# Optimization experiments

Hardware: AMD Instinct MI355X
Metric: run time of the kernel (lower is better)

## Reference

```python
import jax, jax.numpy as jnp
import numpy as np

VOCAB = 50000
EMBED = 256
LABELS = 2
DEPTH = 10          # complete binary tree: 2**DEPTH leaves
B = 256             # batch of trees
L = 2 ** DEPTH      # leaves per tree


def setup_inputs() -> dict:
    key = jax.random.key(0)
    ks = jax.random.split(key, 7)
    token_ids = jax.random.randint(ks[0], (B, L), 0, VOCAB)
    labels = jax.random.randint(ks[1], (B,), 0, LABELS)
    emb = jax.random.normal(ks[2], (VOCAB, EMBED), dtype=jnp.float32)
    W_w = jax.random.normal(ks[3], (EMBED, 2 * EMBED), dtype=jnp.float32) * (1.0 / np.sqrt(2 * EMBED))
    W_b = jax.random.normal(ks[4], (EMBED,), dtype=jnp.float32) * 0.01
    P_w = jax.random.normal(ks[5], (LABELS, EMBED), dtype=jnp.float32) * (1.0 / np.sqrt(EMBED))
    P_b = jax.random.normal(ks[6], (LABELS,), dtype=jnp.float32) * 0.01
    return {"token_ids": token_ids, "labels": labels, "emb": emb,
            "W_w": W_w, "W_b": W_b, "P_w": P_w, "P_b": P_b}


def reference(token_ids, labels, emb, W_w, W_b, P_w, P_b):
    # Leaves: relu(embedding(token))  -> [B, L, E]
    x = jax.nn.relu(emb[token_ids])
    # Level-by-level combine: currentNode = relu(W @ cat(left, right) + b)
    # Leaf order is left-to-right, so adjacent pairs (2k, 2k+1) are siblings;
    # reshape concatenates (left, right) along features, matching torch.cat((l, r), 1).
    while x.shape[1] > 1:
        bsz, n, e = x.shape
        lr = x.reshape(bsz, n // 2, 2 * e)                       # [B, n/2, 2E]
        x = jax.nn.relu(jnp.einsum('bnf,ef->bne', lr, W_w) + W_b)
    root = x[:, 0]                                               # [B, E]
    logits = root @ P_w.T + P_b                                  # [B, label_size]
    prediction = jnp.argmax(logits, axis=1)
    logp = jax.nn.log_softmax(logits, axis=-1)
    loss = -jnp.take_along_axis(logp, labels[:, None], axis=1)[:, 0]  # per-tree CE
    return prediction, loss
```

## Files before the change

kernel.cpp:

```cpp
#include <hip/hip_runtime.h>
#include <hip/hip_bf16.h>
#include <math.h>

#define EMBED   256
#define KDIM    512
#define BATCH   256
#define BM      128
#define BN      128

typedef float  f32x4   __attribute__((ext_vector_type(4)));
typedef __bf16 bf16x8  __attribute__((ext_vector_type(8)));
typedef unsigned short ushort8 __attribute__((ext_vector_type(8)));

__device__ __forceinline__ unsigned short f2h(float f) {
    unsigned int u = __float_as_uint(f);
    u += 0x7FFFu + ((u >> 16) & 1u);
    return (unsigned short)(u >> 16);
}
__device__ __forceinline__ float h2f(unsigned short h) {
    return __uint_as_float(((unsigned int)h) << 16);
}
__device__ __forceinline__ void gload16(const void* g, void* l) {
    __builtin_amdgcn_global_load_lds(
        (const __attribute__((address_space(1))) unsigned int*)g,
        (__attribute__((address_space(3))) unsigned int*)l, 16, 0, 0);
}

template<int LV1, int WPREP>
__global__ __launch_bounds__(256) void gemm_tree(
    const unsigned short* __restrict__ Xh, const unsigned short* __restrict__ Xl,
    const unsigned short* __restrict__ Wh, const unsigned short* __restrict__ Wl,
    const float*  __restrict__ Wf,
    const float*  __restrict__ bias,
    unsigned short* __restrict__ Yh, unsigned short* __restrict__ Yl,
    const int* __restrict__ tok, const float* __restrict__ emb)
{
    __shared__ __align__(16) unsigned short AhL[4096], AlL[4096];
    __shared__ __align__(16) unsigned short BhL[4096], BlL[4096];

    const int tid = threadIdx.x;
    const int w   = tid >> 6;
    const int l   = tid & 63;
    const int q   = l >> 4;
    const int rr  = l & 15;

    const int nwg = gridDim.x;
    const int bid = blockIdx.x;
    const int swz = (bid & 7) * (nwg >> 3) + (bid >> 3);
    const int m0  = (swz >> 1) * BM;
    const int n0  = (swz & 1) * BN;

    const int waveM = w >> 1;
    const int waveN = w & 1;

    int tk[2][2];
    if constexpr (LV1) {
        #pragma unroll
        for (int g = 0; g < 2; ++g) {
            const int r = m0 + (w + g * 4) * 16 + rr;
            tk[g][0] = tok[2 * r];
            tk[g][1] = tok[2 * r + 1];
        }
    }

    f32x4 acc[4][4] = {};

    for (int t = 0; t < 16; ++t) {
        const int k0   = t << 5;
        const int joff = k0 >> 8;
        const int c    = (k0 & 255) + q * 8;

        if constexpr (LV1) {
            #pragma unroll
            for (int g = 0; g < 2; ++g) {
                const int s = w + g * 4;
                const float* e = emb + (size_t)tk[g][joff] * EMBED + c;
                float v[8];
                *(float4*)&v[0] = *(const float4*)e;
                *(float4*)&v[4] = *(const float4*)(e + 4);
                ushort8 hs, ls;
                #pragma unroll
                for (int i = 0; i < 8; ++i) {
                    const float f = fmaxf(v[i], 0.f);
                    const unsigned short h = f2h(f);
                    hs[i] = h;
                    ls[i] = f2h(f - h2f(h));
                }
                *(ushort8*)&AhL[s * 512 + l * 8] = hs;
                *(ushort8*)&AlL[s * 512 + l * 8] = ls;
            }
        } else {
            #pragma unroll
            for (int g = 0; g < 2; ++g) {
                const int s = w + g * 4;
                const size_t off = (size_t)(2 * (m0 + s * 16 + rr) + joff) * EMBED + c;
                gload16(Xh + off, &AhL[s * 512]);
                gload16(Xl + off, &AlL[s * 512]);
            }
        }

        #pragma unroll
        for (int g = 0; g < 2; ++g) {
            const int s = w + g * 4;
            if constexpr (WPREP) {
                const size_t off = (size_t)(n0 + s * 16 + rr) * KDIM + k0 + q * 8;
                gload16(Wh + off, &BhL[s * 512]);
                gload16(Wl + off, &BlL[s * 512]);
            } else {
                const float* ws = Wf + (size_t)(n0 + s * 16 + rr) * KDIM + k0 + q * 8;
                float v[8];
                *(float4*)&v[0] = *(const float4*)ws;
                *(float4*)&v[4] = *(const float4*)(ws + 4);
                ushort8 hs, ls;
                #pragma unroll
                for (int i = 0; i < 8; ++i) {
                    const unsigned short h = f2h(v[i]);
                    hs[i] = h;
                    ls[i] = f2h(v[i] - h2f(h));
                }
                *(ushort8*)&BhL[s * 512 + l * 8] = hs;
                *(ushort8*)&BlL[s * 512 + l * 8] = ls;
            }
        }

        __syncthreads();

        bf16x8 a0[4], b0[4], x0[4];
        #pragma unroll
        for (int mi = 0; mi < 4; ++mi)
            a0[mi] = *(const bf16x8*)&AhL[(waveM * 4 + mi) * 512 + l * 8];
        #pragma unroll
        for (int ni = 0; ni < 4; ++ni)
            b0[ni] = *(const bf16x8*)&BhL[(waveN * 4 + ni) * 512 + l * 8];
        #pragma unroll
        for (int mi = 0; mi < 4; ++mi)
            #pragma unroll
            for (int ni = 0; ni < 4; ++ni)
                acc[mi][ni] = __builtin_amdgcn_mfma_f32_16x16x32_bf16(a0[mi], b0[ni], acc[mi][ni], 0, 0, 0);

        #pragma unroll
        for (int ni = 0; ni < 4; ++ni)
            x0[ni] = *(const bf16x8*)&BlL[(waveN * 4 + ni) * 512 + l * 8];
        #pragma unroll
        for (int mi = 0; mi < 4; ++mi)
            #pragma unroll
            for (int ni = 0; ni < 4; ++ni)
                acc[mi][ni] = __builtin_amdgcn_mfma_f32_16x16x32_bf16(a0[mi], x0[ni], acc[mi][ni], 0, 0, 0);

        #pragma unroll
        for (int mi = 0; mi < 4; ++mi)
            x0[mi] = *(const bf16x8*)&AlL[(waveM * 4 + mi) * 512 + l * 8];
        #pragma unroll
        for (int mi = 0; mi < 4; ++mi)
            #pragma unroll
            for (int ni = 0; ni < 4; ++ni)
                acc[mi][ni] = __builtin_amdgcn_mfma_f32_16x16x32_bf16(x0[mi], b0[ni], acc[mi][ni], 0, 0, 0);

        __syncthreads();
    }

    #pragma unroll
    for (int ni = 0; ni < 4; ++ni) {
        const int col = n0 + waveN * 64 + ni * 16 + rr;
        const float bv = bias[col];
        #pragma unroll
        for (int mi = 0; mi < 4; ++mi) {
            const int row0 = m0 + waveM * 64 + mi * 16 + q * 4;
            #pragma unroll
            for (int jj = 0; jj < 4; ++jj) {
                const float y = fmaxf(acc[mi][ni][jj] + bv, 0.f);
                const unsigned short h = f2h(y);
                Yh[(size_t)(row0 + jj) * EMBED + col] = h;
                Yl[(size_t)(row0 + jj) * EMBED + col] = f2h(y - h2f(h));
            }
        }
    }
}

template<int WPREP>
__global__ __launch_bounds__(256) void tail_kernel(
    const unsigned short* __restrict__ Xh5, const unsigned short* __restrict__ Xl5,
    const unsigned short* __restrict__ Wh, const unsigned short* __restrict__ Wl,
    const float* __restrict__ Wf, const float* __restrict__ bias,
    const float* __restrict__ Pw, const float* __restrict__ Pb,
    const int* __restrict__ labels, float* __restrict__ out)
{
    __shared__ __align__(16) unsigned short X0h[8192], X0l[8192];
    __shared__ __align__(16) unsigned short X1h[4096], X1l[4096];
    __shared__ __align__(16) unsigned short BhT[2][8192], BlT[2][8192];

    const int tid = threadIdx.x;
    const int w   = tid >> 6;
    const int l   = tid & 63;
    const int q   = l >> 4;
    const int rr  = l & 15;
    const int b   = blockIdx.x;

    {
        const int row = tid >> 3;
        const int c0  = (tid & 7) * 32;
        #pragma unroll
        for (int i = 0; i < 4; ++i) {
            const int col = c0 + i * 8;
            const int sw  = (row * 256 + col) ^ ((row & 7) << 3);
            *(ushort8*)&X0h[sw] = *(const ushort8*)&Xh5[(size_t)(b * 32 + row) * EMBED + col];
            *(ushort8*)&X0l[sw] = *(const ushort8*)&Xl5[(size_t)(b * 32 + row) * EMBED + col];
        }
    }

    auto stageB = [&](int buf, int k0) {
        if constexpr (WPREP) {
            #pragma unroll
            for (int j = 0; j < 8; ++j) {
                const int sb = w * 8 + j;
                const int s  = sb & 15;
                const size_t off = (size_t)(s * 16 + rr) * KDIM + k0 + q * 8;
                if (sb < 16) gload16(Wh + off, &BhT[buf][s * 512]);
                else         gload16(Wl + off, &BlT[buf][s * 512]);
            }
        } else {
            #pragma unroll
            for (int j = 0; j < 4; ++j) {
                const int u = w * 4 + j;
                const float* ws = Wf + (size_t)(u * 16 + rr) * KDIM + k0 + q * 8;
                float v[8];
                *(float4*)&v[0] = *(const float4*)ws;
                *(float4*)&v[4] = *(const float4*)(ws + 4);
                ushort8 hs, ls;
                #pragma unroll
                for (int i = 0; i < 8; ++i) {
                    const unsigned short h = f2h(v[i]);
                    hs[i] = h;
                    ls[i] = f2h(v[i] - h2f(h));
                }
                *(ushort8*)&BhT[buf][u * 512 + l * 8] = hs;
                *(ushort8*)&BlT[buf][u * 512 + l * 8] = ls;
            }
        }
    };

    float bv[4];
    #pragma unroll
    for (int ni = 0; ni < 4; ++ni) bv[ni] = bias[w * 64 + ni * 16 + rr];

    stageB(0, 0);
    __syncthreads();

    int g = 0;
    for (int lv = 0; lv < 5; ++lv) {
        unsigned short* srch = (lv & 1) ? X1h : X0h;
        unsigned short* srcl = (lv & 1) ? X1l : X0l;
        unsigned short* dsth = (lv & 1) ? X0h : X1h;
        unsigned short* dstl = (lv & 1) ? X0l : X1l;
        const int Mout = 16 >> lv;

        f32x4 acc[4] = {};
        for (int t = 0; t < 16; ++t, ++g) {
            const int cur = g & 1;
            if (g < 79) stageB(cur ^ 1, ((t + 1) & 15) * 32);

            const int k0   = t * 32;
            const int joff = k0 >> 8;
            const int c    = (k0 & 255) + q * 8;
            const int row  = 2 * rr + joff;
            const int idx  = (row * 256 + c) ^ ((row & 7) << 3);
            const bf16x8 a_h = *(const bf16x8*)&srch[idx];
            const bf16x8 a_l = *(const bf16x8*)&srcl[idx];

            bf16x8 bh4[4], bl4[4];
            #pragma unroll
            for (int ni = 0; ni < 4; ++ni) {
                bh4[ni] = *(const bf16x8*)&BhT[cur][(w * 4 + ni) * 512 + l * 8];
                bl4[ni] = *(const bf16x8*)&BlT[cur][(w * 4 + ni) * 512 + l * 8];
            }
            #pragma unroll
            for (int ni = 0; ni < 4; ++ni)
                acc[ni] = __builtin_amdgcn_mfma_f32_16x16x32_bf16(a_h, bh4[ni], acc[ni], 0, 0, 0);
            #pragma unroll
            for (int ni = 0; ni < 4; ++ni)
                acc[ni] = __builtin_amdgcn_mfma_f32_16x16x32_bf16(a_l, bh4[ni], acc[ni], 0, 0, 0);
            #pragma unroll
            for (int ni = 0; ni < 4; ++ni)
                acc[ni] = __builtin_amdgcn_mfma_f32_16x16x32_bf16(a_h, bl4[ni], acc[ni], 0, 0, 0);

            __syncthreads();
        }

        #pragma unroll
        for (int ni = 0; ni < 4; ++ni) {
            const int col = w * 64 + ni * 16 + rr;
            #pragma unroll
            for (int jj = 0; jj < 4; ++jj) {
                const int row = q * 4 + jj;
                if (row < Mout) {
                    const float y = fmaxf(acc[ni][jj] + bv[ni], 0.f);
                    const unsigned short h = f2h(y);
                    const int idx = (row * 256 + col) ^ ((row & 7) << 3);
                    dsth[idx] = h;
                    dstl[idx] = f2h(y - h2f(h));
                }
            }
        }
        __syncthreads();
    }

    if (w == 0) {
        float s0 = 0.f, s1 = 0.f;
        #pragma unroll
        for (int i = 0; i < 4; ++i) {
            const int col = l + i * 64;
            const float x = h2f(X1h[col]) + h2f(X1l[col]);
            s0 = fmaf(x, Pw[col], s0);
            s1 = fmaf(x, Pw[EMBED + col], s1);
        }
        #pragma unroll
        for (int off = 32; off > 0; off >>= 1) {
            s0 += __shfl_down(s0, off);
            s1 += __shfl_down(s1, off);
        }
        if (l == 0) {
            const float l0 = s0 + Pb[0];
            const float l1 = s1 + Pb[1];
            const int pred = (l1 > l0) ? 1 : 0;
            const float m  = fmaxf(l0, l1);
            const float lse = m + logf(expf(l0 - m) + expf(l1 - m));
            const int lab = labels[b];
            out[b]         = (float)pred;
            out[BATCH + b] = lse - (lab ? l1 : l0);
        }
    }
}

__global__ __launch_bounds__(256) void prep_w(const float* __restrict__ W,
                                              unsigned short* __restrict__ Wh,
                                              unsigned short* __restrict__ Wl)
{
    const int i = blockIdx.x * 256 + threadIdx.x;
    const float w = W[i];
    const unsigned short h = f2h(w);
    Wh[i] = h;
    Wl[i] = f2h(w - h2f(h));
}

extern "C" void kernel_launch(void* const* d_in, const int* in_sizes, int n_in,
                              void* d_out, int out_size, void* d_ws, size_t ws_size,
                              hipStream_t stream)
{
    const int*   token_ids = (const int*)d_in[0];
    const int*   labels    = (const int*)d_in[1];
    const float* emb       = (const float*)d_in[2];
    const float* W_w       = (const float*)d_in[3];
    const float* W_b       = (const float*)d_in[4];
    const float* P_w       = (const float*)d_in[5];
    const float* P_b       = (const float*)d_in[6];
    float*       out       = (float*)d_out;

    unsigned short* Ah_buf = (unsigned short*)d_ws;
    unsigned short* Al_buf = Ah_buf + (size_t)131072 * 256;
    unsigned short* Bh_buf = Al_buf + (size_t)131072 * 256;
    unsigned short* Bl_buf = Bh_buf + (size_t)65536 * 256;
    unsigned short* Wh     = Bl_buf + (size_t)65536 * 256;
    unsigned short* Wl     = Wh + 131072;

    const size_t need_wprep = ((size_t)131072 * 256 * 2 + (size_t)65536 * 256 * 2 + 2 * 131072) * 2;
    const bool wprep = ws_size >= need_wprep;

    if (wprep) prep_w<<<512, 256, 0, stream>>>(W_w, Wh, Wl);

    int R = 131072;
    const unsigned short *inh = nullptr, *inl = nullptr;
    for (int lv = 1; lv <= 5; ++lv) {
        unsigned short* yh = (lv & 1) ? Ah_buf : Bh_buf;
        unsigned short* yl = (lv & 1) ? Al_buf : Bl_buf;
        dim3 grid((R / BM) * 2);
        if (lv == 1) {
            if (wprep) gemm_tree<1,1><<<grid, 256, 0, stream>>>(nullptr, nullptr, Wh, Wl, W_w, W_b, yh, yl, token_ids, emb);
            else       gemm_tree<1,0><<<grid, 256, 0, stream>>>(nullptr, nullptr, Wh, Wl, W_w, W_b, yh, yl, token_ids, emb);
        } else {
            if (wprep) gemm_tree<0,1><<<grid, 256, 0, stream>>>(inh, inl, Wh, Wl, W_w, W_b, yh, yl, nullptr, nullptr);
            else       gemm_tree<0,0><<<grid, 256, 0, stream>>>(inh, inl, Wh, Wl, W_w, W_b, yh, yl, nullptr, nullptr);
        }
        inh = yh; inl = yl; R >>= 1;
    }

    if (wprep) tail_kernel<1><<<BATCH, 256, 0, stream>>>(inh, inl, Wh, Wl, W_w, W_b, P_w, P_b, labels, out);
    else       tail_kernel<0><<<BATCH, 256, 0, stream>>>(inh, inl, Wh, Wl, W_w, W_b, P_w, P_b, labels, out);
}
```

Before: 449.6 us.

## Pre-split embedding table, widen GEMM tiles to full N, fold level five into tail

A new prep kernel converts the ReLU'd embedding table into bf16 hi/lo halves once, so the level-1 GEMM can stage A through direct global-to-LDS loads instead of converting in registers. gemm_tree now uses 512-thread blocks covering all 256 output columns per 128-row tile, so each A tile is read once instead of twice. Level 5 moves into the tail kernel, which streams its 64-row input per tree and runs six levels in one launch, removing a kernel launch and an intermediate round trip. The cost is converting the full 50000x256 table each call, a larger per-block LDS footprint, and reuse of the B buffers as embedding storage.

```diff
diff --git a/kernel.cpp b/kernel.cpp
--- a/kernel.cpp
+++ b/kernel.cpp
@@ -6,7 +6,7 @@
 #define KDIM    512
 #define BATCH   256
 #define BM      128
-#define BN      128
+#define VOCAB   50000
 
 typedef float  f32x4   __attribute__((ext_vector_type(4)));
 typedef __bf16 bf16x8  __attribute__((ext_vector_type(8)));
@@ -26,41 +26,65 @@
         (__attribute__((address_space(3))) unsigned int*)l, 16, 0, 0);
 }
 
+__global__ __launch_bounds__(256) void prep_emb(const float* __restrict__ emb,
+                                                unsigned short* __restrict__ Eh,
+                                                unsigned short* __restrict__ El)
+{
+    const size_t base = ((size_t)blockIdx.x * 256 + threadIdx.x) * 8;
+    float v[8];
+    *(float4*)&v[0] = *(const float4*)&emb[base];
+    *(float4*)&v[4] = *(const float4*)&emb[base + 4];
+    ushort8 hs, ls;
+    #pragma unroll
+    for (int i = 0; i < 8; ++i) {
+        const float f = fmaxf(v[i], 0.f);
+        const unsigned short h = f2h(f);
+        hs[i] = h;
+        ls[i] = f2h(f - h2f(h));
+    }
+    *(ushort8*)&Eh[base] = hs;
+    *(ushort8*)&El[base] = ls;
+}
+
+__global__ __launch_bounds__(256) void prep_w(const float* __restrict__ W,
+                                              unsigned short* __restrict__ Wh,
+                                              unsigned short* __restrict__ Wl)
+{
+    const int i = blockIdx.x * 256 + threadIdx.x;
+    const float w = W[i];
+    const unsigned short h = f2h(w);
+    Wh[i] = h;
+    Wl[i] = f2h(w - h2f(h));
+}
+
 template<int LV1, int WPREP>
-__global__ __launch_bounds__(256) void gemm_tree(
+__global__ __launch_bounds__(512) void gemm_tree(
     const unsigned short* __restrict__ Xh, const unsigned short* __restrict__ Xl,
     const unsigned short* __restrict__ Wh, const unsigned short* __restrict__ Wl,
     const float*  __restrict__ Wf,
     const float*  __restrict__ bias,
     unsigned short* __restrict__ Yh, unsigned short* __restrict__ Yl,
-    const int* __restrict__ tok, const float* __restrict__ emb)
+    const int* __restrict__ tok,
+    const unsigned short* __restrict__ Eh, const unsigned short* __restrict__ El)
 {
     __shared__ __align__(16) unsigned short AhL[4096], AlL[4096];
-    __shared__ __align__(16) unsigned short BhL[4096], BlL[4096];
+    __shared__ __align__(16) unsigned short BhL[8192], BlL[8192];
 
     const int tid = threadIdx.x;
-    const int w   = tid >> 6;
+    const int wid = tid >> 6;
     const int l   = tid & 63;
     const int q   = l >> 4;
     const int rr  = l & 15;
-
-    const int nwg = gridDim.x;
-    const int bid = blockIdx.x;
-    const int swz = (bid & 7) * (nwg >> 3) + (bid >> 3);
-    const int m0  = (swz >> 1) * BM;
-    const int n0  = (swz & 1) * BN;
-
-    const int waveM = w >> 1;
-    const int waveN = w & 1;
-
-    int tk[2][2];
+    const int m0  = blockIdx.x * BM;
+
+    const int waveM = wid >> 2;
+    const int waveN = wid & 3;
+
+    int tk0 = 0, tk1 = 0;
     if constexpr (LV1) {
-        #pragma unroll
-        for (int g = 0; g < 2; ++g) {
-            const int r = m0 + (w + g * 4) * 16 + rr;
-            tk[g][0] = tok[2 * r];
-            tk[g][1] = tok[2 * r + 1];
-        }
+        const int r = m0 + wid * 16 + rr;
+        tk0 = tok[2 * r];
+        tk1 = tok[2 * r + 1];
     }
 
     f32x4 acc[4][4] = {};
@@ -71,43 +95,24 @@
         const int c    = (k0 & 255) + q * 8;
 
         if constexpr (LV1) {
-            #pragma unroll
-            for (int g = 0; g < 2; ++g) {
-                const int s = w + g * 4;
-                const float* e = emb + (size_t)tk[g][joff] * EMBED + c;
-                float v[8];
-                *(float4*)&v[0] = *(const float4*)e;
-                *(float4*)&v[4] = *(const float4*)(e + 4);
-                ushort8 hs, ls;
-                #pragma unroll
-                for (int i = 0; i < 8; ++i) {
-                    const float f = fmaxf(v[i], 0.f);
-                    const unsigned short h = f2h(f);
-                    hs[i] = h;
-                    ls[i] = f2h(f - h2f(h));
-                }
-                *(ushort8*)&AhL[s * 512 + l * 8] = hs;
-                *(ushort8*)&AlL[s * 512 + l * 8] = ls;
-            }
+            const size_t off = (size_t)(joff ? tk1 : tk0) * EMBED + c;
+            gload16(Eh + off, &AhL[wid * 512]);
+            gload16(El + off, &AlL[wid * 512]);
         } else {
-            #pragma unroll
-            for (int g = 0; g < 2; ++g) {
-                const int s = w + g * 4;
-                const size_t off = (size_t)(2 * (m0 + s * 16 + rr) + joff) * EMBED + c;
-                gload16(Xh + off, &AhL[s * 512]);
-                gload16(Xl + off, &AlL[s * 512]);
-            }
+            const size_t off = (size_t)(2 * (m0 + wid * 16 + rr) + joff) * EMBED + c;
+            gload16(Xh + off, &AhL[wid * 512]);
+            gload16(Xl + off, &AlL[wid * 512]);
         }
 
         #pragma unroll
         for (int g = 0; g < 2; ++g) {
-            const int s = w + g * 4;
+            const int s = wid + g * 8;
             if constexpr (WPREP) {
-                const size_t off = (size_t)(n0 + s * 16 + rr) * KDIM + k0 + q * 8;
+                const size_t off = (size_t)(s * 16 + rr) * KDIM + k0 + q * 8;
                 gload16(Wh + off, &BhL[s * 512]);
                 gload16(Wl + off, &BlL[s * 512]);
             } else {
-                const float* ws = Wf + (size_t)(n0 + s * 16 + rr) * KDIM + k0 + q * 8;
+                const float* ws = Wf + (size_t)(s * 16 + rr) * KDIM + k0 + q * 8;
                 float v[8];
                 *(float4*)&v[0] = *(const float4*)ws;
                 *(float4*)&v[4] = *(const float4*)(ws + 4);
@@ -125,43 +130,39 @@
 
         __syncthreads();
 
-        bf16x8 a0[4], b0[4], x0[4];
+        bf16x8 ah[4], al[4], bh[4], bl[4];
+        #pragma unroll
+        for (int mi = 0; mi < 4; ++mi) {
+            ah[mi] = *(const bf16x8*)&AhL[(waveM * 4 + mi) * 512 + l * 8];
+            al[mi] = *(const bf16x8*)&AlL[(waveM * 4 + mi) * 512 + l * 8];
+        }
+        #pragma unroll
+        for (int ni = 0; ni < 4; ++ni) {
+            bh[ni] = *(const bf16x8*)&BhL[(waveN * 4 + ni) * 512 + l * 8];
+            bl[ni] = *(const bf16x8*)&BlL[(waveN * 4 + ni) * 512 + l * 8];
+        }
         #pragma unroll
         for (int mi = 0; mi < 4; ++mi)
-            a0[mi] = *(const bf16x8*)&AhL[(waveM * 4 + mi) * 512 + l * 8];
-        #pragma unroll
-        for (int ni = 0; ni < 4; ++ni)
-            b0[ni] = *(const bf16x8*)&BhL[(waveN * 4 + ni) * 512 + l * 8];
+            #pragma unroll
+            for (int ni = 0; ni < 4; ++ni)
+                acc[mi][ni] = __builtin_amdgcn_mfma_f32_16x16x32_bf16(ah[mi], bh[ni], acc[mi][ni], 0, 0, 0);
         #pragma unroll
         for (int mi = 0; mi < 4; ++mi)
             #pragma unroll
             for (int ni = 0; ni < 4; ++ni)
-                acc[mi][ni] = __builtin_amdgcn_mfma_f32_16x16x32_bf16(a0[mi], b0[ni], acc[mi][ni], 0, 0, 0);
-
-        #pragma unroll
-        for (int ni = 0; ni < 4; ++ni)
-            x0[ni] = *(const bf16x8*)&BlL[(waveN * 4 + ni) * 512 + l * 8];
+                acc[mi][ni] = __builtin_amdgcn_mfma_f32_16x16x32_bf16(al[mi], bh[ni], acc[mi][ni], 0, 0, 0);
         #pragma unroll
         for (int mi = 0; mi < 4; ++mi)
             #pragma unroll
             for (int ni = 0; ni < 4; ++ni)
-                acc[mi][ni] = __builtin_amdgcn_mfma_f32_16x16x32_bf16(a0[mi], x0[ni], acc[mi][ni], 0, 0, 0);
-
-        #pragma unroll
-        for (int mi = 0; mi < 4; ++mi)
-            x0[mi] = *(const bf16x8*)&AlL[(waveM * 4 + mi) * 512 + l * 8];
-        #pragma unroll
-        for (int mi = 0; mi < 4; ++mi)
-            #pragma unroll
-            for (int ni = 0; ni < 4; ++ni)
-                acc[mi][ni] = __builtin_amdgcn_mfma_f32_16x16x32_bf16(x0[mi], b0[ni], acc[mi][ni], 0, 0, 0);
+                acc[mi][ni] = __builtin_amdgcn_mfma_f32_16x16x32_bf16(ah[mi], bl[ni], acc[mi][ni], 0, 0, 0);
 
         __syncthreads();
     }
 
     #pragma unroll
     for (int ni = 0; ni < 4; ++ni) {
-        const int col = n0 + waveN * 64 + ni * 16 + rr;
+        const int col = waveN * 64 + ni * 16 + rr;
         const float bv = bias[col];
         #pragma unroll
         for (int mi = 0; mi < 4; ++mi) {
@@ -179,7 +180,7 @@
 
 template<int WPREP>
 __global__ __launch_bounds__(256) void tail_kernel(
-    const unsigned short* __restrict__ Xh5, const unsigned short* __restrict__ Xl5,
+    const unsigned short* __restrict__ A4h, const unsigned short* __restrict__ A4l,
     const unsigned short* __restrict__ Wh, const unsigned short* __restrict__ Wl,
     const float* __restrict__ Wf, const float* __restrict__ bias,
     const float* __restrict__ Pw, const float* __restrict__ Pb,
@@ -188,6 +189,7 @@
     __shared__ __align__(16) unsigned short X0h[8192], X0l[8192];
     __shared__ __align__(16) unsigned short X1h[4096], X1l[4096];
     __shared__ __align__(16) unsigned short BhT[2][8192], BlT[2][8192];
+    __shared__ __align__(16) unsigned short Asth[2][1024], Astl[2][1024];
 
     const int tid = threadIdx.x;
     const int w   = tid >> 6;
@@ -195,18 +197,6 @@
     const int q   = l >> 4;
     const int rr  = l & 15;
     const int b   = blockIdx.x;
-
-    {
-        const int row = tid >> 3;
-        const int c0  = (tid & 7) * 32;
-        #pragma unroll
-        for (int i = 0; i < 4; ++i) {
-            const int col = c0 + i * 8;
-            const int sw  = (row * 256 + col) ^ ((row & 7) << 3);
-            *(ushort8*)&X0h[sw] = *(const ushort8*)&Xh5[(size_t)(b * 32 + row) * EMBED + col];
-            *(ushort8*)&X0l[sw] = *(const ushort8*)&Xl5[(size_t)(b * 32 + row) * EMBED + col];
-        }
-    }
 
     auto stageB = [&](int buf, int k0) {
         if constexpr (WPREP) {
@@ -239,33 +229,53 @@
         }
     };
 
+    auto stageA = [&](int buf, int t) {
+        if (w < 2) {
+            const int k0   = t * 32;
+            const int joff = k0 >> 8;
+            const int c    = (k0 & 255) + q * 8;
+            const size_t off = (size_t)(64 * b + 2 * (w * 16 + rr) + joff) * EMBED + c;
+            gload16(A4h + off, &Asth[buf][w * 512]);
+            gload16(A4l + off, &Astl[buf][w * 512]);
+        }
+    };
+
     float bv[4];
     #pragma unroll
     for (int ni = 0; ni < 4; ++ni) bv[ni] = bias[w * 64 + ni * 16 + rr];
 
     stageB(0, 0);
+    stageA(0, 0);
     __syncthreads();
 
     int g = 0;
-    for (int lv = 0; lv < 5; ++lv) {
-        unsigned short* srch = (lv & 1) ? X1h : X0h;
-        unsigned short* srcl = (lv & 1) ? X1l : X0l;
-        unsigned short* dsth = (lv & 1) ? X0h : X1h;
-        unsigned short* dstl = (lv & 1) ? X0l : X1l;
-        const int Mout = 16 >> lv;
-
-        f32x4 acc[4] = {};
+    for (int s = 0; s < 6; ++s) {
+        unsigned short* srch = (s & 1) ? X0h : X1h;
+        unsigned short* srcl = (s & 1) ? X0l : X1l;
+        unsigned short* dsth = (s & 1) ? X1h : X0h;
+        unsigned short* dstl = (s & 1) ? X1l : X0l;
+        const int Mout = 32 >> s;
+
+        f32x4 acc[2][4] = {};
         for (int t = 0; t < 16; ++t, ++g) {
             const int cur = g & 1;
-            if (g < 79) stageB(cur ^ 1, ((t + 1) & 15) * 32);
+            if (g < 95) stageB(cur ^ 1, ((t + 1) & 15) * 32);
+            if (s == 0 && t < 15) stageA(cur ^ 1, t + 1);
 
             const int k0   = t * 32;
             const int joff = k0 >> 8;
             const int c    = (k0 & 255) + q * 8;
-            const int row  = 2 * rr + joff;
-            const int idx  = (row * 256 + c) ^ ((row & 7) << 3);
-            const bf16x8 a_h = *(const bf16x8*)&srch[idx];
-            const bf16x8 a_l = *(const bf16x8*)&srcl[idx];
+
+            bf16x8 a_h0, a_l0;
+            if (s == 0) {
+                a_h0 = *(const bf16x8*)&Asth[cur][l * 8];
+                a_l0 = *(const bf16x8*)&Astl[cur][l * 8];
+            } else {
+                const int row = 2 * rr + joff;
+                const int idx = (row * 256 + c) ^ ((row & 7) << 3);
+                a_h0 = *(const bf16x8*)&srch[idx];
+                a_l0 = *(const bf16x8*)&srcl[idx];
+            }
 
             bf16x8 bh4[4], bl4[4];
             #pragma unroll
@@ -275,14 +285,27 @@
             }
             #pragma unroll
             for (int ni = 0; ni < 4; ++ni)
-                acc[ni] = __builtin_amdgcn_mfma_f32_16x16x32_bf16(a_h, bh4[ni], acc[ni], 0, 0, 0);
-            #pragma unroll
-            for (int ni = 0; ni < 4; ++ni)
-                acc[ni] = __builtin_amdgcn_mfma_f32_16x16x32_bf16(a_l, bh4[ni], acc[ni], 0, 0, 0);
-            #pragma unroll
-            for (int ni = 0; ni < 4; ++ni)
-                acc[ni] = __builtin_amdgcn_mfma_f32_16x16x32_bf16(a_h, bl4[ni], acc[ni], 0, 0, 0);
-
+                acc[0][ni] = __builtin_amdgcn_mfma_f32_16x16x32_bf16(a_h0, bh4[ni], acc[0][ni], 0, 0, 0);
+            #pragma unroll
+            for (int ni = 0; ni < 4; ++ni)
+                acc[0][ni] = __builtin_amdgcn_mfma_f32_16x16x32_bf16(a_l0, bh4[ni], acc[0][ni], 0, 0, 0);
+            #pragma unroll
+            for (int ni = 0; ni < 4; ++ni)
+                acc[0][ni] = __builtin_amdgcn_mfma_f32_16x16x32_bf16(a_h0, bl4[ni], acc[0][ni], 0, 0, 0);
+
+            if (s == 0) {
+                const bf16x8 a_h1 = *(const bf16x8*)&Asth[cur][512 + l * 8];
+                const bf16x8 a_l1 = *(const bf16x8*)&Astl[cur][512 + l * 8];
+                #pragma unroll
+                for (int ni = 0; ni < 4; ++ni)
+                    acc[1][ni] = __builtin_amdgcn_mfma_f32_16x16x32_bf16(a_h1, bh4[ni], acc[1][ni], 0, 0, 0);
+                #pragma unroll
+                for (int ni = 0; ni < 4; ++ni)
+                    acc[1][ni] = __builtin_amdgcn_mfma_f32_16x16x32_bf16(a_l1, bh4[ni], acc[1][ni], 0, 0, 0);
+                #pragma unroll
+                for (int ni = 0; ni < 4; ++ni)
+                    acc[1][ni] = __builtin_amdgcn_mfma_f32_16x16x32_bf16(a_h1, bl4[ni], acc[1][ni], 0, 0, 0);
+            }
             __syncthreads();
         }
 
@@ -293,7 +316,18 @@
             for (int jj = 0; jj < 4; ++jj) {
                 const int row = q * 4 + jj;
                 if (row < Mout) {
-                    const float y = fmaxf(acc[ni][jj] + bv[ni], 0.f);
+                    const float y = fmaxf(acc[0][ni][jj] + bv[ni], 0.f);
+                    const unsigned short h = f2h(y);
+                    const int idx = (row * 256 + col) ^ ((row & 7) << 3);
+                    dsth[idx] = h;
+                    dstl[idx] = f2h(y - h2f(h));
+                }
+            }
+            if (s == 0) {
+                #pragma unroll
+                for (int jj = 0; jj < 4; ++jj) {
+                    const int row = 16 + q * 4 + jj;
+                    const float y = fmaxf(acc[1][ni][jj] + bv[ni], 0.f);
                     const unsigned short h = f2h(y);
                     const int idx = (row * 256 + col) ^ ((row & 7) << 3);
                     dsth[idx] = h;
@@ -329,17 +363,6 @@
             out[BATCH + b] = lse - (lab ? l1 : l0);
         }
     }
-}
-
-__global__ __launch_bounds__(256) void prep_w(const float* __restrict__ W,
-                                              unsigned short* __restrict__ Wh,
-                                              unsigned short* __restrict__ Wl)
-{
-    const int i = blockIdx.x * 256 + threadIdx.x;
-    const float w = W[i];
-    const unsigned short h = f2h(w);
-    Wh[i] = h;
-    Wl[i] = f2h(w - h2f(h));
 }
 
 extern "C" void kernel_launch(void* const* d_in, const int* in_sizes, int n_in,
@@ -361,28 +384,26 @@
     unsigned short* Bl_buf = Bh_buf + (size_t)65536 * 256;
     unsigned short* Wh     = Bl_buf + (size_t)65536 * 256;
     unsigned short* Wl     = Wh + 131072;
+    unsigned short* Eh     = Bh_buf;
+    unsigned short* El     = Bl_buf;
 
     const size_t need_wprep = ((size_t)131072 * 256 * 2 + (size_t)65536 * 256 * 2 + 2 * 131072) * 2;
     const bool wprep = ws_size >= need_wprep;
 
     if (wprep) prep_w<<<512, 256, 0, stream>>>(W_w, Wh, Wl);
-
-    int R = 131072;
-    const unsigned short *inh = nullptr, *inl = nullptr;
-    for (int lv = 1; lv <= 5; ++lv) {
-        unsigned short* yh = (lv & 1) ? Ah_buf : Bh_buf;
-        unsigned short* yl = (lv & 1) ? Al_buf : Bl_buf;
-        dim3 grid((R / BM) * 2);
-        if (lv == 1) {
-            if (wprep) gemm_tree<1,1><<<grid, 256, 0, stream>>>(nullptr, nullptr, Wh, Wl, W_w, W_b, yh, yl, token_ids, emb);
-            else       gemm_tree<1,0><<<grid, 256, 0, stream>>>(nullptr, nullptr, Wh, Wl, W_w, W_b, yh, yl, token_ids, emb);
-        } else {
-            if (wprep) gemm_tree<0,1><<<grid, 256, 0, stream>>>(inh, inl, Wh, Wl, W_w, W_b, yh, yl, nullptr, nullptr);
-            else       gemm_tree<0,0><<<grid, 256, 0, stream>>>(inh, inl, Wh, Wl, W_w, W_b, yh, yl, nullptr, nullptr);
-        }
-        inh = yh; inl = yl; R >>= 1;
-    }
-
-    if (wprep) tail_kernel<1><<<BATCH, 256, 0, stream>>>(inh, inl, Wh, Wl, W_w, W_b, P_w, P_b, labels, out);
-    else       tail_kernel<0><<<BATCH, 256, 0, stream>>>(inh, inl, Wh, Wl, W_w, W_b, P_w, P_b, labels, out);
-}
+    prep_emb<<<(VOCAB * EMBED) / 2048, 256, 0, stream>>>(emb, Eh, El);
+
+    if (wprep) {
+        gemm_tree<1,1><<<1024, 512, 0, stream>>>(nullptr, nullptr, Wh, Wl, W_w, W_b, Ah_buf, Al_buf, token_ids, Eh, El);
+        gemm_tree<0,1><<< 512, 512, 0, stream>>>(Ah_buf, Al_buf, Wh, Wl, W_w, W_b, Bh_buf, Bl_buf, nullptr, nullptr, nullptr);
+        gemm_tree<0,1><<< 256, 512, 0, stream>>>(Bh_buf, Bl_buf, Wh, Wl, W_w, W_b, Ah_buf, Al_buf, nullptr, nullptr, nullptr);
+        gemm_tree<0,1><<< 128, 512, 0, stream>>>(Ah_buf, Al_buf, Wh, Wl, W_w, W_b, Bh_buf, Bl_buf, nullptr, nullptr, nullptr);
+        tail_kernel<1><<<BATCH, 256, 0, stream>>>(Bh_buf, Bl_buf, Wh, Wl, W_w, W_b, P_w, P_b, labels, out);
+    } else {
+        gemm_tree<1,0><<<1024, 512, 0, stream>>>(nullptr, nullptr, Wh, Wl, W_w, W_b, Ah_buf, Al_buf, token_ids, Eh, El);
+        gemm_tree<0,0><<< 512, 512, 0, stream>>>(Ah_buf, Al_buf, Wh, Wl, W_w, W_b, Bh_buf, Bl_buf, nullptr, nullptr, nullptr);
+        gemm_tree<0,0><<< 256, 512, 0, stream>>>(Bh_buf, Bl_buf, Wh, Wl, W_w, W_b, Ah_buf, Al_buf, nullptr, nullptr, nullptr);
+        gemm_tree<0,0><<< 128, 512, 0, stream>>>(Ah_buf, Al_buf, Wh, Wl, W_w, W_b, Bh_buf, Bl_buf, nullptr, nullptr, nullptr);
+        tail_kernel<0><<<BATCH, 256, 0, stream>>>(Bh_buf, Bl_buf, Wh, Wl, W_w, W_b, P_w, P_b, labels, out);
+    }
+}
```

Result: no change. 452.0 us (+0.5%).
